# Optimization experiments

Measured on AMD Instinct MI355X. Metric: run time of the kernel, lower is better.

## Reference

```python
import jax, jax.numpy as jnp
import numpy as np

N_NODES = 50000
N_EDGES = 800000
IN_F, HID, OUT = 128, 128, 64


def setup_inputs() -> dict:
    key = jax.random.key(0)
    ks = jax.random.split(key, 12)
    sc = 0.05
    return {
        "features": jax.random.normal(ks[0], (N_NODES, IN_F), jnp.float32),
        "src": jax.random.randint(ks[1], (N_EDGES,), 0, N_NODES, jnp.int32),
        "dst": jax.random.randint(ks[2], (N_EDGES,), 0, N_NODES, jnp.int32),
        "Wself0": jax.random.normal(ks[3], (IN_F, HID), jnp.float32) * sc,
        "Wneigh0": jax.random.normal(ks[4], (IN_F, HID), jnp.float32) * sc,
        "b0": jnp.zeros((HID,), jnp.float32),
        "Wself1": jax.random.normal(ks[5], (HID, HID), jnp.float32) * sc,
        "Wneigh1": jax.random.normal(ks[6], (HID, HID), jnp.float32) * sc,
        "b1": jnp.zeros((HID,), jnp.float32),
        "Wself2": jax.random.normal(ks[7], (HID, OUT), jnp.float32) * sc,
        "Wneigh2": jax.random.normal(ks[8], (HID, OUT), jnp.float32) * sc,
        "b2": jnp.zeros((OUT,), jnp.float32),
    }


def _sage_conv(h, src, dst, Ws, Wn, b, act):
    # mean aggregator: mean over in-neighbors (src -> dst), zero for isolated nodes
    msg = h[src]                                            # [E, d] gather
    agg = jax.ops.segment_sum(msg, dst, num_segments=N_NODES)
    deg = jax.ops.segment_sum(jnp.ones((msg.shape[0],), h.dtype), dst,
                              num_segments=N_NODES)
    mean = agg / jnp.maximum(deg, 1.0)[:, None]             # [N, d]
    out = h @ Ws + mean @ Wn + b                            # fc_self + fc_neigh + bias
    return jax.nn.relu(out) if act else out


def reference(features, src, dst, Wself0, Wneigh0, b0, Wself1, Wneigh1, b1,
              Wself2, Wneigh2, b2):
    h = _sage_conv(features, src, dst, Wself0, Wneigh0, b0, True)
    h = _sage_conv(h, src, dst, Wself1, Wneigh1, b1, True)
    h = _sage_conv(h, src, dst, Wself2, Wneigh2, b2, False)
    return h
```

## Files before the change

kernel.cpp:

```cpp
#include <hip/hip_runtime.h>
#include <hip/hip_fp16.h>

#define N_NODES_C 50000
#define N_EDGES_C 800000
#define K_FEAT 128
#define HM_STRIDE 256
#define NB_C 196

typedef unsigned int uint_t;
typedef _Float16 half8 __attribute__((ext_vector_type(8)));
typedef _Float16 half4 __attribute__((ext_vector_type(4)));
typedef float f32x4 __attribute__((ext_vector_type(4)));


__global__ __launch_bounds__(256) void p1hist_kernel(const int* __restrict__ dst,
                                                     uint_t* __restrict__ histG, int E) {
    __shared__ uint_t hist[256];
    const int t = threadIdx.x, b = blockIdx.x;
    hist[t] = 0;
    __syncthreads();
    const int base = b * 4096;
#pragma unroll
    for (int j = 0; j < 16; ++j) {
        int idx = base + t + j * 256;
        if (idx < E) atomicAdd(&hist[((uint_t)dst[idx]) >> 8], 1u);
    }
    __syncthreads();
    histG[b * 256 + t] = hist[t];
}

__global__ __launch_bounds__(256) void p1scan_kernel(uint_t* __restrict__ histG,
                                                     uint_t* __restrict__ cbase) {
    const int t = threadIdx.x;
    uint_t run = 0;
    for (int bb = 0; bb < NB_C; bb += 28) {
        uint_t vals[28];
#pragma unroll
        for (int j = 0; j < 28; ++j) vals[j] = histG[(size_t)(bb + j) * 256 + t];
#pragma unroll
        for (int j = 0; j < 28; ++j) {
            uint_t x = vals[j];
            vals[j] = run;
            run += x;
        }
#pragma unroll
        for (int j = 0; j < 28; ++j) histG[(size_t)(bb + j) * 256 + t] = vals[j];
    }
    const int lane = t & 63, wid = t >> 6;
    uint_t x = run;
#pragma unroll
    for (int off = 1; off < 64; off <<= 1) {
        uint_t y = __shfl_up(x, off, 64);
        if (lane >= off) x += y;
    }
    __shared__ uint_t wsum[4];
    if (lane == 63) wsum[wid] = x;
    __syncthreads();
    uint_t wpre = 0;
#pragma unroll
    for (int w = 0; w < 4; ++w)
        if (w < wid) wpre += wsum[w];
    uint_t incl = wpre + x;
    cbase[t] = incl - run;
    if (t == 255) cbase[256] = incl;
}

__global__ __launch_bounds__(256) void p1scatter_kernel(const int* __restrict__ src,
                                                        const int* __restrict__ dst,
                                                        const uint_t* __restrict__ histG,
                                                        const uint_t* __restrict__ cbase,
                                                        uint_t* __restrict__ tmp, int E) {
    __shared__ uint_t cur[256];
    const int t = threadIdx.x, b = blockIdx.x;
    cur[t] = histG[b * 256 + t] + cbase[t];
    __syncthreads();
    const int base = b * 4096;
#pragma unroll
    for (int j = 0; j < 16; ++j) {
        int idx = base + t + j * 256;
        if (idx < E) {
            uint_t d = (uint_t)dst[idx];
            uint_t s = (uint_t)src[idx];
            uint_t slot = atomicAdd(&cur[d >> 8], 1u);
            tmp[slot] = ((d & 255u) << 16) | s;
        }
    }
}

__global__ __launch_bounds__(256) void p2_kernel(const uint_t* __restrict__ tmp,
                                                 const uint_t* __restrict__ cbase,
                                                 int* __restrict__ offs, int* __restrict__ ssrc) {
    __shared__ uint_t hist[256];
    __shared__ uint_t cur[256];
    __shared__ uint_t wsum[4];
    const int t = threadIdx.x, c = blockIdx.x;
    const uint_t cb = cbase[c], ce = cbase[c + 1];
    hist[t] = 0;
    __syncthreads();
    for (uint_t i = cb + t; i < ce; i += 256) atomicAdd(&hist[tmp[i] >> 16], 1u);
    __syncthreads();
    const uint_t v = hist[t];
    const int lane = t & 63, wid = t >> 6;
    uint_t x = v;
#pragma unroll
    for (int off = 1; off < 64; off <<= 1) {
        uint_t y = __shfl_up(x, off, 64);
        if (lane >= off) x += y;
    }
    if (lane == 63) wsum[wid] = x;
    __syncthreads();
    uint_t wpre = 0;
#pragma unroll
    for (int w = 0; w < 4; ++w)
        if (w < wid) wpre += wsum[w];
    const uint_t excl = wpre + x - v;
    const int node = c * 256 + t;
    if (node < N_NODES_C) offs[node] = (int)(cb + excl);
    if (c == 0 && t == 0) offs[N_NODES_C] = N_EDGES_C;
    cur[t] = excl;
    __syncthreads();
    for (uint_t i = cb + t; i < ce; i += 256) {
        uint_t p = tmp[i];
        uint_t slot = cb + atomicAdd(&cur[p >> 16], 1u);
        ssrc[slot] = (int)(p & 0xFFFFu);
    }
}


__global__ __launch_bounds__(256) void convert_kernel(
    const float* __restrict__ feat, _Float16* __restrict__ hm0,
    const float* __restrict__ Ws0, const float* __restrict__ Wn0,
    const float* __restrict__ Ws1, const float* __restrict__ Wn1,
    const float* __restrict__ Ws2, const float* __restrict__ Wn2,
    _Float16* __restrict__ WT0, _Float16* __restrict__ WT1, _Float16* __restrict__ WT2) {
    const int i = blockIdx.x * 256 + threadIdx.x;
    const int n4 = N_NODES_C * K_FEAT / 4;
    if (i < n4) {
        float4 v = reinterpret_cast<const float4*>(feat)[i];
        int n = i >> 5, c4 = i & 31;
        half4 o;
        o.x = (_Float16)v.x; o.y = (_Float16)v.y; o.z = (_Float16)v.z; o.w = (_Float16)v.w;
        *reinterpret_cast<half4*>(hm0 + (size_t)n * HM_STRIDE + c4 * 4) = o;
    } else {
        int idx = i - n4;
        if (idx >= 81920) return;
        const float* Ws;
        const float* Wn;
        _Float16* WT;
        int ncol;
        if (idx < 32768) { Ws = Ws0; Wn = Wn0; WT = WT0; ncol = 128; }
        else if (idx < 65536) { idx -= 32768; Ws = Ws1; Wn = Wn1; WT = WT1; ncol = 128; }
        else { idx -= 65536; Ws = Ws2; Wn = Wn2; WT = WT2; ncol = 64; }
        int k = idx & 255, c = idx >> 8;
        float v = (k < 128) ? Ws[(size_t)k * ncol + c] : Wn[(size_t)(k - 128) * ncol + c];
        WT[(size_t)c * 256 + k] = (_Float16)v;
    }
}


__global__ void mean_kernel(_Float16* __restrict__ hm, const int* __restrict__ offs,
                            const int* __restrict__ ssrc) {
    const int node = (int)((blockIdx.x * blockDim.x + threadIdx.x) >> 6);
    const int lane = threadIdx.x & 63;
    if (node >= N_NODES_C) return;
    const int beg = offs[node], end = offs[node + 1];
    const int g = lane >> 4;
    const int cb = (lane & 15) * 8;
    const _Float16* base = hm + cb;

    float accA[8] = {0.f, 0.f, 0.f, 0.f, 0.f, 0.f, 0.f, 0.f};
    float accB[8] = {0.f, 0.f, 0.f, 0.f, 0.f, 0.f, 0.f, 0.f};

    int e = beg;
    for (; e + 8 <= end; e += 8) {
        const int s0 = ssrc[e + g];
        const int s1 = ssrc[e + 4 + g];
        half8 v0 = *reinterpret_cast<const half8*>(base + (size_t)s0 * HM_STRIDE);
        half8 v1 = *reinterpret_cast<const half8*>(base + (size_t)s1 * HM_STRIDE);
#pragma unroll
        for (int j = 0; j < 8; ++j) accA[j] += (float)v0[j];
#pragma unroll
        for (int j = 0; j < 8; ++j) accB[j] += (float)v1[j];
    }
    for (; e + 4 <= end; e += 4) {
        const int s0 = ssrc[e + g];
        half8 v0 = *reinterpret_cast<const half8*>(base + (size_t)s0 * HM_STRIDE);
#pragma unroll
        for (int j = 0; j < 8; ++j) accA[j] += (float)v0[j];
    }
    if (e < end) {
        const bool valid = (e + g) < end;
        const int s0 = valid ? ssrc[e + g] : ssrc[beg];
        half8 v0 = *reinterpret_cast<const half8*>(base + (size_t)s0 * HM_STRIDE);
        if (valid) {
#pragma unroll
            for (int j = 0; j < 8; ++j) accB[j] += (float)v0[j];
        }
    }

    const float inv = (end > beg) ? 1.0f / (float)(end - beg) : 0.f;
    half8 o;
#pragma unroll
    for (int j = 0; j < 8; ++j) {
        float x = accA[j] + accB[j];
        x += __shfl_xor(x, 16, 64);
        x += __shfl_xor(x, 32, 64);
        o[j] = (_Float16)(x * inv);
    }
    if (lane < 16)
        *reinterpret_cast<half8*>(hm + (size_t)node * HM_STRIDE + 128 + cb) = o;
}


template <int NCOL, bool ACT, bool OUT_FP32>
__global__ __launch_bounds__(256) void sage_mfma(
    const _Float16* __restrict__ hm,
    const _Float16* __restrict__ WT,
    const float* __restrict__ bias,
    float* __restrict__ outf,
    _Float16* __restrict__ outh,
    int nNodes) {
    constexpr int CF = NCOL / 16;
    constexpr int RPW = 32;
    constexpr int RPB = 128;

    __shared__ _Float16 bl[NCOL][256];

    const int t = threadIdx.x;
#pragma unroll
    for (int it = 0; it < NCOL * 32 / 256; ++it) {
        int f = t + it * 256;
        int row = f >> 5, c8 = f & 31;
        half8 v = *reinterpret_cast<const half8*>(WT + (size_t)row * 256 + c8 * 8);
        int col = (c8 * 8) ^ ((row & 7) << 3);
        *reinterpret_cast<half8*>(&bl[row][col]) = v;
    }
    __syncthreads();

    const int wid = t >> 6;
    const int lane = t & 63;
    const int r0 = blockIdx.x * RPB + wid * RPW;
    const int koff = (lane >> 4) * 8;

    half8 a[2][8];
#pragma unroll
    for (int fr = 0; fr < 2; ++fr) {
        int row = r0 + fr * 16 + (lane & 15);
        if (row >= nNodes) row = nNodes - 1;
        const _Float16* ap = hm + (size_t)row * HM_STRIDE + koff;
#pragma unroll
        for (int ks = 0; ks < 8; ++ks)
            a[fr][ks] = *reinterpret_cast<const half8*>(ap + ks * 32);
    }

    f32x4 acc[2][CF];
#pragma unroll
    for (int fr = 0; fr < 2; ++fr)
#pragma unroll
        for (int c = 0; c < CF; ++c) acc[fr][c] = {0.f, 0.f, 0.f, 0.f};

#pragma unroll
    for (int c = 0; c < CF; ++c) {
        const int brow = c * 16 + (lane & 15);
        const int bswz = (brow & 7) << 3;
#pragma unroll
        for (int ks = 0; ks < 8; ++ks) {
            half8 b = *reinterpret_cast<const half8*>(&bl[brow][(ks * 32 + koff) ^ bswz]);
            acc[0][c] = __builtin_amdgcn_mfma_f32_16x16x32_f16(a[0][ks], b, acc[0][c], 0, 0, 0);
            acc[1][c] = __builtin_amdgcn_mfma_f32_16x16x32_f16(a[1][ks], b, acc[1][c], 0, 0, 0);
        }
    }

    const int ocol = lane & 15;
    const int orow_off = (lane >> 4) << 2;
#pragma unroll
    for (int fr = 0; fr < 2; ++fr) {
        const int rbase = r0 + fr * 16 + orow_off;
#pragma unroll
        for (int c = 0; c < CF; ++c) {
            const int col = c * 16 + ocol;
            const float bv = bias[col];
#pragma unroll
            for (int reg = 0; reg < 4; ++reg) {
                const int row = rbase + reg;
                if (row < nNodes) {
                    float v = acc[fr][c][reg] + bv;
                    if (ACT) v = fmaxf(v, 0.f);
                    if (OUT_FP32) outf[(size_t)row * NCOL + col] = v;
                    else outh[(size_t)row * HM_STRIDE + col] = (_Float16)v;
                }
            }
        }
    }
}


extern "C" void kernel_launch(void* const* d_in, const int* in_sizes, int n_in,
                              void* d_out, int out_size, void* d_ws, size_t ws_size,
                              hipStream_t stream) {
    const float* feat = (const float*)d_in[0];
    const int* src = (const int*)d_in[1];
    const int* dst = (const int*)d_in[2];
    const float* Ws0 = (const float*)d_in[3];
    const float* Wn0 = (const float*)d_in[4];
    const float* b0 = (const float*)d_in[5];
    const float* Ws1 = (const float*)d_in[6];
    const float* Wn1 = (const float*)d_in[7];
    const float* b1 = (const float*)d_in[8];
    const float* Ws2 = (const float*)d_in[9];
    const float* Wn2 = (const float*)d_in[10];
    const float* b2 = (const float*)d_in[11];
    float* out = (float*)d_out;

    auto align_up = [](size_t x) { return (x + 255) & ~(size_t)255; };
    char* w = (char*)d_ws;
    uint_t* histG = (uint_t*)w; w += align_up((size_t)NB_C * 256 * 4);
    uint_t* cbase = (uint_t*)w; w += align_up(257 * 4);
    uint_t* tmp = (uint_t*)w;   w += align_up((size_t)N_EDGES_C * 4);
    int* offs = (int*)w;        w += align_up((size_t)(N_NODES_C + 1) * 4);
    int* ssrc = (int*)w;        w += align_up((size_t)N_EDGES_C * 4);
    _Float16* hm0 = (_Float16*)w; w += align_up((size_t)N_NODES_C * HM_STRIDE * 2);
    _Float16* hm1 = (_Float16*)w; w += align_up((size_t)N_NODES_C * HM_STRIDE * 2);
    _Float16* WT0 = (_Float16*)w; w += align_up((size_t)128 * 256 * 2);
    _Float16* WT1 = (_Float16*)w; w += align_up((size_t)128 * 256 * 2);
    _Float16* WT2 = (_Float16*)w; w += align_up((size_t)64 * 256 * 2);
    _Float16* hm2 = hm0;

    p1hist_kernel<<<NB_C, 256, 0, stream>>>(dst, histG, N_EDGES_C);
    p1scan_kernel<<<1, 256, 0, stream>>>(histG, cbase);
    p1scatter_kernel<<<NB_C, 256, 0, stream>>>(src, dst, histG, cbase, tmp, N_EDGES_C);
    p2_kernel<<<NB_C, 256, 0, stream>>>(tmp, cbase, offs, ssrc);

    const int convBlocks = (N_NODES_C * K_FEAT / 4 + 81920 + 255) / 256;
    convert_kernel<<<convBlocks, 256, 0, stream>>>(
        feat, hm0, Ws0, Wn0, Ws1, Wn1, Ws2, Wn2, WT0, WT1, WT2);

    const int meanBlocks = (N_NODES_C * 64 + 255) / 256;
    const int gemmBlocks = (N_NODES_C + 127) / 128;

    mean_kernel<<<meanBlocks, 256, 0, stream>>>(hm0, offs, ssrc);
    sage_mfma<128, true, false><<<gemmBlocks, 256, 0, stream>>>(
        hm0, WT0, b0, nullptr, hm1, N_NODES_C);

    mean_kernel<<<meanBlocks, 256, 0, stream>>>(hm1, offs, ssrc);
    sage_mfma<128, true, false><<<gemmBlocks, 256, 0, stream>>>(
        hm1, WT1, b1, nullptr, hm2, N_NODES_C);

    mean_kernel<<<meanBlocks, 256, 0, stream>>>(hm2, offs, ssrc);
    sage_mfma<64, false, true><<<gemmBlocks, 256, 0, stream>>>(
        hm2, WT2, b2, out, nullptr, N_NODES_C);
}
```

Measured before the change: 173.3 us.

## Split mean aggregation into column-slice passes and fuse conversion into histogram

The mean aggregation now runs as four column passes. Each block handles a 32-column slice of the feature row, so each lane reads a 4-byte half2 instead of a 16-byte half8. The idea is to shrink the gathered working set per pass so the randomly accessed rows of the feature matrix stay in cache. The cost is that the index list and offsets are read four times, and each gather moves fewer bytes. Separately, the feature and weight fp16 conversion is merged into the histogram launch to save one kernel launch, and the index loads and output stores use nontemporal hints.

New measurement: 346.7 us. +100.0%, slower.

```diff
diff --git a/kernel.cpp b/kernel.cpp
--- a/kernel.cpp
+++ b/kernel.cpp
@@ -6,6 +6,7 @@
 #define K_FEAT 128
 #define HM_STRIDE 256
 #define NB_C 196
+#define MEAN_NB (N_NODES_C / 4)
 
 typedef unsigned int uint_t;
 typedef _Float16 half8 __attribute__((ext_vector_type(8)));
@@ -13,20 +14,50 @@
 typedef float f32x4 __attribute__((ext_vector_type(4)));
 
 
-__global__ __launch_bounds__(256) void p1hist_kernel(const int* __restrict__ dst,
-                                                     uint_t* __restrict__ histG, int E) {
-    __shared__ uint_t hist[256];
+__global__ __launch_bounds__(256) void p1hist_conv_kernel(
+    const int* __restrict__ dst, uint_t* __restrict__ histG, int E,
+    const float* __restrict__ feat, _Float16* __restrict__ hm0,
+    const float* __restrict__ Ws0, const float* __restrict__ Wn0,
+    const float* __restrict__ Ws1, const float* __restrict__ Wn1,
+    const float* __restrict__ Ws2, const float* __restrict__ Wn2,
+    _Float16* __restrict__ WT0, _Float16* __restrict__ WT1, _Float16* __restrict__ WT2) {
     const int t = threadIdx.x, b = blockIdx.x;
-    hist[t] = 0;
-    __syncthreads();
-    const int base = b * 4096;
-#pragma unroll
-    for (int j = 0; j < 16; ++j) {
-        int idx = base + t + j * 256;
-        if (idx < E) atomicAdd(&hist[((uint_t)dst[idx]) >> 8], 1u);
-    }
-    __syncthreads();
-    histG[b * 256 + t] = hist[t];
+    if (b < NB_C) {
+        __shared__ uint_t hist[256];
+        hist[t] = 0;
+        __syncthreads();
+        const int base = b * 4096;
+#pragma unroll
+        for (int j = 0; j < 16; ++j) {
+            int idx = base + t + j * 256;
+            if (idx < E) atomicAdd(&hist[((uint_t)dst[idx]) >> 8], 1u);
+        }
+        __syncthreads();
+        histG[b * 256 + t] = hist[t];
+    } else {
+        const int i = (b - NB_C) * 256 + t;
+        const int n4 = N_NODES_C * K_FEAT / 4;
+        if (i < n4) {
+            float4 v = reinterpret_cast<const float4*>(feat)[i];
+            int n = i >> 5, c4 = i & 31;
+            half4 o;
+            o.x = (_Float16)v.x; o.y = (_Float16)v.y; o.z = (_Float16)v.z; o.w = (_Float16)v.w;
+            *reinterpret_cast<half4*>(hm0 + (size_t)n * HM_STRIDE + c4 * 4) = o;
+        } else {
+            int idx = i - n4;
+            if (idx >= 81920) return;
+            const float* Ws;
+            const float* Wn;
+            _Float16* WT;
+            int ncol;
+            if (idx < 32768) { Ws = Ws0; Wn = Wn0; WT = WT0; ncol = 128; }
+            else if (idx < 65536) { idx -= 32768; Ws = Ws1; Wn = Wn1; WT = WT1; ncol = 128; }
+            else { idx -= 65536; Ws = Ws2; Wn = Wn2; WT = WT2; ncol = 64; }
+            int k = idx & 255, c = idx >> 8;
+            float v = (k < 128) ? Ws[(size_t)k * ncol + c] : Wn[(size_t)(k - 128) * ncol + c];
+            WT[(size_t)c * 256 + k] = (_Float16)v;
+        }
+    }
 }
 
 __global__ __launch_bounds__(256) void p1scan_kernel(uint_t* __restrict__ histG,
@@ -127,88 +158,57 @@
 }
 
 
-__global__ __launch_bounds__(256) void convert_kernel(
-    const float* __restrict__ feat, _Float16* __restrict__ hm0,
-    const float* __restrict__ Ws0, const float* __restrict__ Wn0,
-    const float* __restrict__ Ws1, const float* __restrict__ Wn1,
-    const float* __restrict__ Ws2, const float* __restrict__ Wn2,
-    _Float16* __restrict__ WT0, _Float16* __restrict__ WT1, _Float16* __restrict__ WT2) {
-    const int i = blockIdx.x * 256 + threadIdx.x;
-    const int n4 = N_NODES_C * K_FEAT / 4;
-    if (i < n4) {
-        float4 v = reinterpret_cast<const float4*>(feat)[i];
-        int n = i >> 5, c4 = i & 31;
-        half4 o;
-        o.x = (_Float16)v.x; o.y = (_Float16)v.y; o.z = (_Float16)v.z; o.w = (_Float16)v.w;
-        *reinterpret_cast<half4*>(hm0 + (size_t)n * HM_STRIDE + c4 * 4) = o;
-    } else {
-        int idx = i - n4;
-        if (idx >= 81920) return;
-        const float* Ws;
-        const float* Wn;
-        _Float16* WT;
-        int ncol;
-        if (idx < 32768) { Ws = Ws0; Wn = Wn0; WT = WT0; ncol = 128; }
-        else if (idx < 65536) { idx -= 32768; Ws = Ws1; Wn = Wn1; WT = WT1; ncol = 128; }
-        else { idx -= 65536; Ws = Ws2; Wn = Wn2; WT = WT2; ncol = 64; }
-        int k = idx & 255, c = idx >> 8;
-        float v = (k < 128) ? Ws[(size_t)k * ncol + c] : Wn[(size_t)(k - 128) * ncol + c];
-        WT[(size_t)c * 256 + k] = (_Float16)v;
-    }
-}
-
-
-__global__ void mean_kernel(_Float16* __restrict__ hm, const int* __restrict__ offs,
-                            const int* __restrict__ ssrc) {
-    const int node = (int)((blockIdx.x * blockDim.x + threadIdx.x) >> 6);
+__global__ __launch_bounds__(256) void mean_pass_kernel(_Float16* __restrict__ hm,
+                                                        const int* __restrict__ offs,
+                                                        const int* __restrict__ ssrc) {
+    const int blk = blockIdx.x;
+    const int pass = blk / MEAN_NB;
+    const int nb = blk - pass * MEAN_NB;
+    const int wid = threadIdx.x >> 6;
+    const int node = nb * 4 + wid;
     const int lane = threadIdx.x & 63;
-    if (node >= N_NODES_C) return;
+    const int g = lane >> 4;
+    const int c = lane & 15;
     const int beg = offs[node], end = offs[node + 1];
-    const int g = lane >> 4;
-    const int cb = (lane & 15) * 8;
-    const _Float16* base = hm + cb;
-
-    float accA[8] = {0.f, 0.f, 0.f, 0.f, 0.f, 0.f, 0.f, 0.f};
-    float accB[8] = {0.f, 0.f, 0.f, 0.f, 0.f, 0.f, 0.f, 0.f};
-
+    const _Float16* base = hm + pass * 32 + c * 2;
+
+    float a0A = 0.f, a1A = 0.f, a0B = 0.f, a1B = 0.f;
     int e = beg;
     for (; e + 8 <= end; e += 8) {
-        const int s0 = ssrc[e + g];
-        const int s1 = ssrc[e + 4 + g];
-        half8 v0 = *reinterpret_cast<const half8*>(base + (size_t)s0 * HM_STRIDE);
-        half8 v1 = *reinterpret_cast<const half8*>(base + (size_t)s1 * HM_STRIDE);
-#pragma unroll
-        for (int j = 0; j < 8; ++j) accA[j] += (float)v0[j];
-#pragma unroll
-        for (int j = 0; j < 8; ++j) accB[j] += (float)v1[j];
+        const int s0 = __builtin_nontemporal_load(ssrc + e + g);
+        const int s1 = __builtin_nontemporal_load(ssrc + e + 4 + g);
+        float2 v0 = __half22float2(*reinterpret_cast<const __half2*>(base + (size_t)s0 * HM_STRIDE));
+        float2 v1 = __half22float2(*reinterpret_cast<const __half2*>(base + (size_t)s1 * HM_STRIDE));
+        a0A += v0.x; a1A += v0.y;
+        a0B += v1.x; a1B += v1.y;
     }
     for (; e + 4 <= end; e += 4) {
-        const int s0 = ssrc[e + g];
-        half8 v0 = *reinterpret_cast<const half8*>(base + (size_t)s0 * HM_STRIDE);
-#pragma unroll
-        for (int j = 0; j < 8; ++j) accA[j] += (float)v0[j];
+        const int s0 = __builtin_nontemporal_load(ssrc + e + g);
+        float2 v0 = __half22float2(*reinterpret_cast<const __half2*>(base + (size_t)s0 * HM_STRIDE));
+        a0A += v0.x; a1A += v0.y;
     }
     if (e < end) {
         const bool valid = (e + g) < end;
         const int s0 = valid ? ssrc[e + g] : ssrc[beg];
-        half8 v0 = *reinterpret_cast<const half8*>(base + (size_t)s0 * HM_STRIDE);
-        if (valid) {
-#pragma unroll
-            for (int j = 0; j < 8; ++j) accB[j] += (float)v0[j];
-        }
-    }
-
-    const float inv = (end > beg) ? 1.0f / (float)(end - beg) : 0.f;
-    half8 o;
-#pragma unroll
-    for (int j = 0; j < 8; ++j) {
-        float x = accA[j] + accB[j];
-        x += __shfl_xor(x, 16, 64);
-        x += __shfl_xor(x, 32, 64);
-        o[j] = (_Float16)(x * inv);
-    }
-    if (lane < 16)
-        *reinterpret_cast<half8*>(hm + (size_t)node * HM_STRIDE + 128 + cb) = o;
+        float2 v0 = __half22float2(*reinterpret_cast<const __half2*>(base + (size_t)s0 * HM_STRIDE));
+        if (valid) { a0B += v0.x; a1B += v0.y; }
+    }
+
+    float x0 = a0A + a0B, x1 = a1A + a1B;
+    x0 += __shfl_xor(x0, 16, 64);
+    x0 += __shfl_xor(x0, 32, 64);
+    x1 += __shfl_xor(x1, 16, 64);
+    x1 += __shfl_xor(x1, 32, 64);
+    if (lane < 16) {
+        const float inv = (end > beg) ? 1.0f / (float)(end - beg) : 0.f;
+        float2 m;
+        m.x = x0 * inv;
+        m.y = x1 * inv;
+        __half2 o = __float22half2_rn(m);
+        __builtin_nontemporal_store(
+            *reinterpret_cast<uint_t*>(&o),
+            reinterpret_cast<uint_t*>(hm + (size_t)node * HM_STRIDE + 128 + pass * 32 + c * 2));
+    }
 }
 
 
@@ -326,27 +326,25 @@
     _Float16* WT2 = (_Float16*)w; w += align_up((size_t)64 * 256 * 2);
     _Float16* hm2 = hm0;
 
-    p1hist_kernel<<<NB_C, 256, 0, stream>>>(dst, histG, N_EDGES_C);
+    const int convBlocks = (N_NODES_C * K_FEAT / 4 + 81920 + 255) / 256;
+    p1hist_conv_kernel<<<NB_C + convBlocks, 256, 0, stream>>>(
+        dst, histG, N_EDGES_C, feat, hm0, Ws0, Wn0, Ws1, Wn1, Ws2, Wn2, WT0, WT1, WT2);
     p1scan_kernel<<<1, 256, 0, stream>>>(histG, cbase);
     p1scatter_kernel<<<NB_C, 256, 0, stream>>>(src, dst, histG, cbase, tmp, N_EDGES_C);
     p2_kernel<<<NB_C, 256, 0, stream>>>(tmp, cbase, offs, ssrc);
 
-    const int convBlocks = (N_NODES_C * K_FEAT / 4 + 81920 + 255) / 256;
-    convert_kernel<<<convBlocks, 256, 0, stream>>>(
-        feat, hm0, Ws0, Wn0, Ws1, Wn1, Ws2, Wn2, WT0, WT1, WT2);
-
-    const int meanBlocks = (N_NODES_C * 64 + 255) / 256;
+    const int meanBlocks = MEAN_NB * 4;
     const int gemmBlocks = (N_NODES_C + 127) / 128;
 
-    mean_kernel<<<meanBlocks, 256, 0, stream>>>(hm0, offs, ssrc);
+    mean_pass_kernel<<<meanBlocks, 256, 0, stream>>>(hm0, offs, ssrc);
     sage_mfma<128, true, false><<<gemmBlocks, 256, 0, stream>>>(
         hm0, WT0, b0, nullptr, hm1, N_NODES_C);
 
-    mean_kernel<<<meanBlocks, 256, 0, stream>>>(hm1, offs, ssrc);
+    mean_pass_kernel<<<meanBlocks, 256, 0, stream>>>(hm1, offs, ssrc);
     sage_mfma<128, true, false><<<gemmBlocks, 256, 0, stream>>>(
         hm1, WT1, b1, nullptr, hm2, N_NODES_C);
 
-    mean_kernel<<<meanBlocks, 256, 0, stream>>>(hm2, offs, ssrc);
+    mean_pass_kernel<<<meanBlocks, 256, 0, stream>>>(hm2, offs, ssrc);
     sage_mfma<64, false, true><<<gemmBlocks, 256, 0, stream>>>(
         hm2, WT2, b2, out, nullptr, N_NODES_C);
 }
```

## Split node features into 32-column slabs for cache-local mean gathers

Applied to the files above, without the earlier changes.

Stores hidden features as four column slabs of 32 halves per node (each slab about 3.2MB), and the mean kernel runs one pass per slab. Each pass's random gathers then touch a smaller working set that may stay in L2/MALL. The mean output moves to a separate buffer, and the GEMM reads its A operand from both the slab layout and that buffer. The histogram and fp16 convert kernels are also merged into one launch. In exchange, gathers are narrower (8-byte loads), need an extra shuffle-reduction step, and the whole edge list is re-read four times per layer.

After: 275.5 us. 59.0% more time.

```diff
diff --git a/kernel.cpp b/kernel.cpp
--- a/kernel.cpp
+++ b/kernel.cpp
@@ -4,8 +4,8 @@
 #define N_NODES_C 50000
 #define N_EDGES_C 800000
 #define K_FEAT 128
-#define HM_STRIDE 256
 #define NB_C 196
+#define MEAN_NB (N_NODES_C / 4)
 
 typedef unsigned int uint_t;
 typedef _Float16 half8 __attribute__((ext_vector_type(8)));
@@ -13,20 +13,52 @@
 typedef float f32x4 __attribute__((ext_vector_type(4)));
 
 
-__global__ __launch_bounds__(256) void p1hist_kernel(const int* __restrict__ dst,
-                                                     uint_t* __restrict__ histG, int E) {
-    __shared__ uint_t hist[256];
+
+__global__ __launch_bounds__(256) void p1hist_conv_kernel(
+    const int* __restrict__ dst, uint_t* __restrict__ histG, int E,
+    const float* __restrict__ feat, _Float16* __restrict__ hs0,
+    const float* __restrict__ Ws0, const float* __restrict__ Wn0,
+    const float* __restrict__ Ws1, const float* __restrict__ Wn1,
+    const float* __restrict__ Ws2, const float* __restrict__ Wn2,
+    _Float16* __restrict__ WT0, _Float16* __restrict__ WT1, _Float16* __restrict__ WT2) {
     const int t = threadIdx.x, b = blockIdx.x;
-    hist[t] = 0;
-    __syncthreads();
-    const int base = b * 4096;
-#pragma unroll
-    for (int j = 0; j < 16; ++j) {
-        int idx = base + t + j * 256;
-        if (idx < E) atomicAdd(&hist[((uint_t)dst[idx]) >> 8], 1u);
-    }
-    __syncthreads();
-    histG[b * 256 + t] = hist[t];
+    if (b < NB_C) {
+        __shared__ uint_t hist[256];
+        hist[t] = 0;
+        __syncthreads();
+        const int base = b * 4096;
+#pragma unroll
+        for (int j = 0; j < 16; ++j) {
+            int idx = base + t + j * 256;
+            if (idx < E) atomicAdd(&hist[((uint_t)dst[idx]) >> 8], 1u);
+        }
+        __syncthreads();
+        histG[b * 256 + t] = hist[t];
+    } else {
+        const int i = (b - NB_C) * 256 + t;
+        const int n4 = N_NODES_C * K_FEAT / 4;
+        if (i < n4) {
+            float4 v = reinterpret_cast<const float4*>(feat)[i];
+            int n = i >> 5, c4 = i & 31;
+            int p = c4 >> 3, cc = (c4 & 7) * 4;
+            half4 o;
+            o.x = (_Float16)v.x; o.y = (_Float16)v.y; o.z = (_Float16)v.z; o.w = (_Float16)v.w;
+            *reinterpret_cast<half4*>(hs0 + ((size_t)p * N_NODES_C + n) * 32 + cc) = o;
+        } else {
+            int idx = i - n4;
+            if (idx >= 81920) return;
+            const float* Ws;
+            const float* Wn;
+            _Float16* WT;
+            int ncol;
+            if (idx < 32768) { Ws = Ws0; Wn = Wn0; WT = WT0; ncol = 128; }
+            else if (idx < 65536) { idx -= 32768; Ws = Ws1; Wn = Wn1; WT = WT1; ncol = 128; }
+            else { idx -= 65536; Ws = Ws2; Wn = Wn2; WT = WT2; ncol = 64; }
+            int k = idx & 255, c = idx >> 8;
+            float v = (k < 128) ? Ws[(size_t)k * ncol + c] : Wn[(size_t)(k - 128) * ncol + c];
+            WT[(size_t)c * 256 + k] = (_Float16)v;
+        }
+    }
 }
 
 __global__ __launch_bounds__(256) void p1scan_kernel(uint_t* __restrict__ histG,
@@ -127,101 +159,74 @@
 }
 
 
-__global__ __launch_bounds__(256) void convert_kernel(
-    const float* __restrict__ feat, _Float16* __restrict__ hm0,
-    const float* __restrict__ Ws0, const float* __restrict__ Wn0,
-    const float* __restrict__ Ws1, const float* __restrict__ Wn1,
-    const float* __restrict__ Ws2, const float* __restrict__ Wn2,
-    _Float16* __restrict__ WT0, _Float16* __restrict__ WT1, _Float16* __restrict__ WT2) {
-    const int i = blockIdx.x * 256 + threadIdx.x;
-    const int n4 = N_NODES_C * K_FEAT / 4;
-    if (i < n4) {
-        float4 v = reinterpret_cast<const float4*>(feat)[i];
-        int n = i >> 5, c4 = i & 31;
-        half4 o;
-        o.x = (_Float16)v.x; o.y = (_Float16)v.y; o.z = (_Float16)v.z; o.w = (_Float16)v.w;
-        *reinterpret_cast<half4*>(hm0 + (size_t)n * HM_STRIDE + c4 * 4) = o;
-    } else {
-        int idx = i - n4;
-        if (idx >= 81920) return;
-        const float* Ws;
-        const float* Wn;
-        _Float16* WT;
-        int ncol;
-        if (idx < 32768) { Ws = Ws0; Wn = Wn0; WT = WT0; ncol = 128; }
-        else if (idx < 65536) { idx -= 32768; Ws = Ws1; Wn = Wn1; WT = WT1; ncol = 128; }
-        else { idx -= 65536; Ws = Ws2; Wn = Wn2; WT = WT2; ncol = 64; }
-        int k = idx & 255, c = idx >> 8;
-        float v = (k < 128) ? Ws[(size_t)k * ncol + c] : Wn[(size_t)(k - 128) * ncol + c];
-        WT[(size_t)c * 256 + k] = (_Float16)v;
-    }
-}
-
-
-__global__ void mean_kernel(_Float16* __restrict__ hm, const int* __restrict__ offs,
-                            const int* __restrict__ ssrc) {
-    const int node = (int)((blockIdx.x * blockDim.x + threadIdx.x) >> 6);
+__global__ __launch_bounds__(256) void mean_pass_kernel(const _Float16* __restrict__ hs,
+                                                        _Float16* __restrict__ mb,
+                                                        const int* __restrict__ offs,
+                                                        const int* __restrict__ ssrc) {
+    const int blk = blockIdx.x;
+    const int pass = blk / MEAN_NB;
+    const int nb = blk - pass * MEAN_NB;
+    const int node = nb * 4 + (threadIdx.x >> 6);
     const int lane = threadIdx.x & 63;
-    if (node >= N_NODES_C) return;
+    const int g = lane >> 3;
+    const int c4 = (lane & 7) * 4;
+    const _Float16* base = hs + (size_t)pass * N_NODES_C * 32 + c4;
     const int beg = offs[node], end = offs[node + 1];
-    const int g = lane >> 4;
-    const int cb = (lane & 15) * 8;
-    const _Float16* base = hm + cb;
-
-    float accA[8] = {0.f, 0.f, 0.f, 0.f, 0.f, 0.f, 0.f, 0.f};
-    float accB[8] = {0.f, 0.f, 0.f, 0.f, 0.f, 0.f, 0.f, 0.f};
-
+
+    float a0[4] = {0.f, 0.f, 0.f, 0.f};
+    float a1[4] = {0.f, 0.f, 0.f, 0.f};
     int e = beg;
+    for (; e + 16 <= end; e += 16) {
+        const int s0 = ssrc[e + g];
+        const int s1 = ssrc[e + 8 + g];
+        half4 v0 = *reinterpret_cast<const half4*>(base + (size_t)s0 * 32);
+        half4 v1 = *reinterpret_cast<const half4*>(base + (size_t)s1 * 32);
+#pragma unroll
+        for (int j = 0; j < 4; ++j) a0[j] += (float)v0[j];
+#pragma unroll
+        for (int j = 0; j < 4; ++j) a1[j] += (float)v1[j];
+    }
     for (; e + 8 <= end; e += 8) {
         const int s0 = ssrc[e + g];
-        const int s1 = ssrc[e + 4 + g];
-        half8 v0 = *reinterpret_cast<const half8*>(base + (size_t)s0 * HM_STRIDE);
-        half8 v1 = *reinterpret_cast<const half8*>(base + (size_t)s1 * HM_STRIDE);
-#pragma unroll
-        for (int j = 0; j < 8; ++j) accA[j] += (float)v0[j];
-#pragma unroll
-        for (int j = 0; j < 8; ++j) accB[j] += (float)v1[j];
-    }
-    for (; e + 4 <= end; e += 4) {
-        const int s0 = ssrc[e + g];
-        half8 v0 = *reinterpret_cast<const half8*>(base + (size_t)s0 * HM_STRIDE);
-#pragma unroll
-        for (int j = 0; j < 8; ++j) accA[j] += (float)v0[j];
+        half4 v0 = *reinterpret_cast<const half4*>(base + (size_t)s0 * 32);
+#pragma unroll
+        for (int j = 0; j < 4; ++j) a0[j] += (float)v0[j];
     }
     if (e < end) {
         const bool valid = (e + g) < end;
         const int s0 = valid ? ssrc[e + g] : ssrc[beg];
-        half8 v0 = *reinterpret_cast<const half8*>(base + (size_t)s0 * HM_STRIDE);
+        half4 v0 = *reinterpret_cast<const half4*>(base + (size_t)s0 * 32);
         if (valid) {
 #pragma unroll
-            for (int j = 0; j < 8; ++j) accB[j] += (float)v0[j];
+            for (int j = 0; j < 4; ++j) a1[j] += (float)v0[j];
         }
     }
 
     const float inv = (end > beg) ? 1.0f / (float)(end - beg) : 0.f;
-    half8 o;
-#pragma unroll
-    for (int j = 0; j < 8; ++j) {
-        float x = accA[j] + accB[j];
+    half4 o;
+#pragma unroll
+    for (int j = 0; j < 4; ++j) {
+        float x = a0[j] + a1[j];
+        x += __shfl_xor(x, 8, 64);
         x += __shfl_xor(x, 16, 64);
         x += __shfl_xor(x, 32, 64);
         o[j] = (_Float16)(x * inv);
     }
-    if (lane < 16)
-        *reinterpret_cast<half8*>(hm + (size_t)node * HM_STRIDE + 128 + cb) = o;
+    if (lane < 8)
+        *reinterpret_cast<half4*>(mb + (size_t)node * 128 + pass * 32 + c4) = o;
 }
 
 
 template <int NCOL, bool ACT, bool OUT_FP32>
 __global__ __launch_bounds__(256) void sage_mfma(
-    const _Float16* __restrict__ hm,
+    const _Float16* __restrict__ hs,
+    const _Float16* __restrict__ mb,
     const _Float16* __restrict__ WT,
     const float* __restrict__ bias,
     float* __restrict__ outf,
     _Float16* __restrict__ outh,
     int nNodes) {
     constexpr int CF = NCOL / 16;
-    constexpr int RPW = 32;
     constexpr int RPB = 128;
 
     __shared__ _Float16 bl[NCOL][256];
@@ -239,7 +244,7 @@
 
     const int wid = t >> 6;
     const int lane = t & 63;
-    const int r0 = blockIdx.x * RPB + wid * RPW;
+    const int r0 = blockIdx.x * RPB + wid * 32;
     const int koff = (lane >> 4) * 8;
 
     half8 a[2][8];
@@ -247,10 +252,14 @@
     for (int fr = 0; fr < 2; ++fr) {
         int row = r0 + fr * 16 + (lane & 15);
         if (row >= nNodes) row = nNodes - 1;
-        const _Float16* ap = hm + (size_t)row * HM_STRIDE + koff;
-#pragma unroll
-        for (int ks = 0; ks < 8; ++ks)
-            a[fr][ks] = *reinterpret_cast<const half8*>(ap + ks * 32);
+#pragma unroll
+        for (int ks = 0; ks < 4; ++ks)
+            a[fr][ks] = *reinterpret_cast<const half8*>(
+                hs + ((size_t)ks * N_NODES_C + row) * 32 + koff);
+#pragma unroll
+        for (int ks = 4; ks < 8; ++ks)
+            a[fr][ks] = *reinterpret_cast<const half8*>(
+                mb + (size_t)row * 128 + (ks - 4) * 32 + koff);
     }
 
     f32x4 acc[2][CF];
@@ -280,6 +289,7 @@
         for (int c = 0; c < CF; ++c) {
             const int col = c * 16 + ocol;
             const float bv = bias[col];
+            const int sp = col >> 5, scc = col & 31;
 #pragma unroll
             for (int reg = 0; reg < 4; ++reg) {
                 const int row = rbase + reg;
@@ -287,7 +297,7 @@
                     float v = acc[fr][c][reg] + bv;
                     if (ACT) v = fmaxf(v, 0.f);
                     if (OUT_FP32) outf[(size_t)row * NCOL + col] = v;
-                    else outh[(size_t)row * HM_STRIDE + col] = (_Float16)v;
+                    else outh[((size_t)sp * N_NODES_C + row) * 32 + scc] = (_Float16)v;
                 }
             }
         }
@@ -319,34 +329,32 @@
     uint_t* tmp = (uint_t*)w;   w += align_up((size_t)N_EDGES_C * 4);
     int* offs = (int*)w;        w += align_up((size_t)(N_NODES_C + 1) * 4);
     int* ssrc = (int*)w;        w += align_up((size_t)N_EDGES_C * 4);
-    _Float16* hm0 = (_Float16*)w; w += align_up((size_t)N_NODES_C * HM_STRIDE * 2);
-    _Float16* hm1 = (_Float16*)w; w += align_up((size_t)N_NODES_C * HM_STRIDE * 2);
+    _Float16* hsA = (_Float16*)w; w += align_up((size_t)4 * N_NODES_C * 32 * 2);
+    _Float16* hsB = (_Float16*)w; w += align_up((size_t)4 * N_NODES_C * 32 * 2);
+    _Float16* mb = (_Float16*)w;  w += align_up((size_t)N_NODES_C * 128 * 2);
     _Float16* WT0 = (_Float16*)w; w += align_up((size_t)128 * 256 * 2);
     _Float16* WT1 = (_Float16*)w; w += align_up((size_t)128 * 256 * 2);
     _Float16* WT2 = (_Float16*)w; w += align_up((size_t)64 * 256 * 2);
-    _Float16* hm2 = hm0;
-
-    p1hist_kernel<<<NB_C, 256, 0, stream>>>(dst, histG, N_EDGES_C);
+
+    const int convBlocks = (N_NODES_C * K_FEAT / 4 + 81920 + 255) / 256;
+    p1hist_conv_kernel<<<NB_C + convBlocks, 256, 0, stream>>>(
+        dst, histG, N_EDGES_C, feat, hsA, Ws0, Wn0, Ws1, Wn1, Ws2, Wn2, WT0, WT1, WT2);
     p1scan_kernel<<<1, 256, 0, stream>>>(histG, cbase);
     p1scatter_kernel<<<NB_C, 256, 0, stream>>>(src, dst, histG, cbase, tmp, N_EDGES_C);
     p2_kernel<<<NB_C, 256, 0, stream>>>(tmp, cbase, offs, ssrc);
 
-    const int convBlocks = (N_NODES_C * K_FEAT / 4 + 81920 + 255) / 256;
-    convert_kernel<<<convBlocks, 256, 0, stream>>>(
-        feat, hm0, Ws0, Wn0, Ws1, Wn1, Ws2, Wn2, WT0, WT1, WT2);
-
-    const int meanBlocks = (N_NODES_C * 64 + 255) / 256;
+    const int meanBlocks = MEAN_NB * 4;
     const int gemmBlocks = (N_NODES_C + 127) / 128;
 
-    mean_kernel<<<meanBlocks, 256, 0, stream>>>(hm0, offs, ssrc);
+    mean_pass_kernel<<<meanBlocks, 256, 0, stream>>>(hsA, mb, offs, ssrc);
     sage_mfma<128, true, false><<<gemmBlocks, 256, 0, stream>>>(
-        hm0, WT0, b0, nullptr, hm1, N_NODES_C);
-
-    mean_kernel<<<meanBlocks, 256, 0, stream>>>(hm1, offs, ssrc);
+        hsA, mb, WT0, b0, nullptr, hsB, N_NODES_C);
+
+    mean_pass_kernel<<<meanBlocks, 256, 0, stream>>>(hsB, mb, offs, ssrc);
     sage_mfma<128, true, false><<<gemmBlocks, 256, 0, stream>>>(
-        hm1, WT1, b1, nullptr, hm2, N_NODES_C);
-
-    mean_kernel<<<meanBlocks, 256, 0, stream>>>(hm2, offs, ssrc);
+        hsB, mb, WT1, b1, nullptr, hsA, N_NODES_C);
+
+    mean_pass_kernel<<<meanBlocks, 256, 0, stream>>>(hsA, mb, offs, ssrc);
     sage_mfma<64, false, true><<<gemmBlocks, 256, 0, stream>>>(
-        hm2, WT2, b2, out, nullptr, N_NODES_C);
-}
+        hsA, mb, WT2, b2, out, nullptr, N_NODES_C);
+}
```
